# Kernel optimization log

Measured on AMD Instinct MI355X. Metric: run time of the kernel, lower is better.

The kernel has to match this reference:

```python
import jax, jax.numpy as jnp
import numpy as np

S = 4096  # source_sequence_size
Q = 4096  # query_sequence_size
E = 2048  # embedding_size
D = 2048  # output_embedding_size


def setup_inputs() -> dict:
    key = jax.random.key(0)
    ks = jax.random.split(key, 9)
    s = 1.0 / np.sqrt(E)
    return {
        "key": jax.random.normal(ks[0], (S, E), jnp.float32),
        "value": jax.random.normal(ks[1], (S, E), jnp.float32),
        "query": jax.random.normal(ks[2], (Q, E), jnp.float32),
        "Wk": jax.random.normal(ks[3], (D, E), jnp.float32) * s,
        "bk": jax.random.normal(ks[4], (D,), jnp.float32) * 0.01,
        "Wq": jax.random.normal(ks[5], (D, E), jnp.float32) * s,
        "bq": jax.random.normal(ks[6], (D,), jnp.float32) * 0.01,
        "Wv": jax.random.normal(ks[7], (D, E), jnp.float32) * s,
        "bv": jax.random.normal(ks[8], (D,), jnp.float32) * 0.01,
    }


def reference(key, value, query, Wk, bk, Wq, bq, Wv, bv):
    # Linear projections (nn.Linear: x @ W.T + b)
    k = key @ Wk.T + bk      # [S, D]
    v = value @ Wv.T + bv    # [S, D]
    q = query @ Wq.T + bq    # [Q, D]
    # Per-query-token attention scores over all source tokens (schema BOTH),
    # then weighted sum over value rows -- vectorized form of the per-token
    # apply_attention_scores loop.
    scale = 1.0 / jnp.sqrt(jnp.asarray(D, q.dtype))
    scores = jax.nn.softmax(jnp.einsum("qd,sd->qs", q, k) * scale, axis=-1)  # [Q, S]
    return jnp.einsum("qs,sd->qd", scores, v)  # [Q, D]
```

## Files before the change

kernel.cpp:

```cpp
#include <hip/hip_runtime.h>

#define S_SEQ 4096
#define Q_SEQ 4096
#define E_DIM 2048
#define D_DIM 2048

typedef __bf16 bf16;
typedef __bf16 bf16x4 __attribute__((ext_vector_type(4)));
typedef __bf16 bf16x8 __attribute__((ext_vector_type(8)));
typedef float f32x4 __attribute__((ext_vector_type(4)));

__global__ __launch_bounds__(256) void cast6(
    const float* __restrict__ i0, const float* __restrict__ i1,
    const float* __restrict__ i2, const float* __restrict__ i3,
    const float* __restrict__ i4, const float* __restrict__ i5,
    bf16* __restrict__ o0, bf16* __restrict__ o1, bf16* __restrict__ o2,
    bf16* __restrict__ o3, bf16* __restrict__ o4, bf16* __restrict__ o5) {
  const float* in;
  bf16* out;
  int n4;
  switch (blockIdx.y) {
    case 0: in = i0; out = o0; n4 = (S_SEQ * E_DIM) / 4; break;
    case 1: in = i1; out = o1; n4 = (S_SEQ * E_DIM) / 4; break;
    case 2: in = i2; out = o2; n4 = (S_SEQ * E_DIM) / 4; break;
    case 3: in = i3; out = o3; n4 = (D_DIM * E_DIM) / 4; break;
    case 4: in = i4; out = o4; n4 = (D_DIM * E_DIM) / 4; break;
    default: in = i5; out = o5; n4 = (D_DIM * E_DIM) / 4; break;
  }
  int i = blockIdx.x * 256 + threadIdx.x;
  if (i < n4) {
    float4 v = reinterpret_cast<const float4*>(in)[i];
    bf16x4 o;
    o[0] = (bf16)v.x; o[1] = (bf16)v.y; o[2] = (bf16)v.z; o[3] = (bf16)v.w;
    *reinterpret_cast<bf16x4*>(out + 4 * (size_t)i) = o;
  }
}

__device__ __forceinline__ void async_copy16(const bf16* g, bf16* l) {
  __builtin_amdgcn_global_load_lds(
      (const __attribute__((address_space(1))) void*)g,
      (__attribute__((address_space(3))) void*)l, 16, 0, 0);
}

__device__ __forceinline__ void xcd_remap32(int id, int nt, int& m, int& n) {
  int xcd = id & 7;
  int lid = id >> 3;
  m = (xcd & 3) * 8 + (lid & 7);
  n = (xcd >> 2) * (nt >> 1) + (lid >> 3);
}
__device__ __forceinline__ void xcd_remap16(int id, int nt, int& m, int& n) {
  int xcd = id & 7;
  int lid = id >> 3;
  m = (xcd & 3) * 4 + (lid & 3);
  n = (xcd >> 2) * (nt >> 1) + (lid >> 2);
}

template <int EPI>
__device__ __forceinline__ void gemm_body_sb(
    const bf16* __restrict__ A, int lda,
    const bf16* __restrict__ B, int ldb,
    void* __restrict__ C, int ldc,
    const float* __restrict__ aux, float scale, int K, int mBase, int nBase) {
  __shared__ __align__(16) bf16 Als[128 * 64];
  __shared__ __align__(16) bf16 Bls[128 * 64];

  const int tid  = threadIdx.x;
  const int wave = tid >> 6;
  const int lane = tid & 63;
  const int quad = lane >> 4;
  const int lrow = lane & 15;
  const int wRow = (wave >> 1) * 64;
  const int wCol = (wave & 1) * 64;

  f32x4 acc[4][4];
#pragma unroll
  for (int i = 0; i < 4; ++i)
#pragma unroll
    for (int j = 0; j < 4; ++j) {
      f32x4 z = {0.f, 0.f, 0.f, 0.f};
      acc[i][j] = z;
    }

  for (int k0 = 0; k0 < K; k0 += 64) {
#pragma unroll
    for (int c = 0; c < 4; ++c) {
      int chunk = c * 256 + tid;
      int row = chunk >> 3;
      int kc = (chunk & 7) ^ (row & 7);
      const bf16* g = A + (size_t)(mBase + row) * lda + k0 + kc * 8;
      async_copy16(g, Als + (size_t)(c * 256 + wave * 64) * 8);
    }
#pragma unroll
    for (int c = 0; c < 4; ++c) {
      int chunk = c * 256 + tid;
      int row = chunk >> 3;
      int kc = (chunk & 7) ^ (row & 7);
      const bf16* g = B + (size_t)(nBase + row) * ldb + k0 + kc * 8;
      async_copy16(g, Bls + (size_t)(c * 256 + wave * 64) * 8);
    }
    __syncthreads();

#pragma unroll
    for (int kk = 0; kk < 2; ++kk) {
      bf16x8 af[4], bfr[4];
#pragma unroll
      for (int i = 0; i < 4; ++i) {
        int r = wRow + i * 16 + lrow;
        int slot = (kk * 4 + quad) ^ (r & 7);
        af[i] = *(const bf16x8*)(Als + (size_t)r * 64 + slot * 8);
      }
#pragma unroll
      for (int j = 0; j < 4; ++j) {
        int r = wCol + j * 16 + lrow;
        int slot = (kk * 4 + quad) ^ (r & 7);
        bfr[j] = *(const bf16x8*)(Bls + (size_t)r * 64 + slot * 8);
      }
#pragma unroll
      for (int i = 0; i < 4; ++i)
#pragma unroll
        for (int j = 0; j < 4; ++j)
          acc[i][j] = __builtin_amdgcn_mfma_f32_16x16x32_bf16(af[i], bfr[j], acc[i][j], 0, 0, 0);
    }
    __syncthreads();
  }

#pragma unroll
  for (int j = 0; j < 4; ++j) {
    const int cn = nBase + wCol + j * 16 + lrow;
    float bj = 0.f;
    if (EPI == 0) bj = aux[cn];
#pragma unroll
    for (int i = 0; i < 4; ++i) {
      const int rbase = mBase + wRow + i * 16 + quad * 4;
#pragma unroll
      for (int r = 0; r < 4; ++r) {
        if (EPI == 0)
          ((bf16*)C)[(size_t)(rbase + r) * ldc + cn] = (bf16)(acc[i][j][r] + bj);
      }
    }
  }
}

template <int EPI>
__device__ __forceinline__ void gemm_body_c(
    const bf16* __restrict__ A, int lda,
    const bf16* __restrict__ B, int ldb,
    void* __restrict__ C, int ldc,
    float scale, int K, int mBase, int nBase,
    float* __restrict__ psum) {
  __shared__ __align__(16) bf16 Als[256 * 64];
  __shared__ __align__(16) bf16 Bls[128 * 64];

  const int tid  = threadIdx.x;
  const int wave = tid >> 6;
  const int lane = tid & 63;
  const int quad = lane >> 4;
  const int lrow = lane & 15;
  const int wRow = (wave >> 1) * 128;
  const int wCol = (wave & 1) * 64;

  f32x4 acc[8][4];
#pragma unroll
  for (int i = 0; i < 8; ++i)
#pragma unroll
    for (int j = 0; j < 4; ++j) {
      f32x4 z = {0.f, 0.f, 0.f, 0.f};
      acc[i][j] = z;
    }

  for (int k0 = 0; k0 < K; k0 += 64) {
#pragma unroll
    for (int c = 0; c < 8; ++c) {
      int chunk = c * 256 + tid;
      int row = chunk >> 3;
      int kc = (chunk & 7) ^ (row & 7);
      const bf16* g = A + (size_t)(mBase + row) * lda + k0 + kc * 8;
      async_copy16(g, Als + (size_t)(c * 256 + wave * 64) * 8);
    }
#pragma unroll
    for (int c = 0; c < 4; ++c) {
      int chunk = c * 256 + tid;
      int row = chunk >> 3;
      int kc = (chunk & 7) ^ (row & 7);
      const bf16* g = B + (size_t)(nBase + row) * ldb + k0 + kc * 8;
      async_copy16(g, Bls + (size_t)(c * 256 + wave * 64) * 8);
    }
    __syncthreads();

#pragma unroll
    for (int kk = 0; kk < 2; ++kk) {
      bf16x8 af[8], bfr[4];
#pragma unroll
      for (int i = 0; i < 8; ++i) {
        int r = wRow + i * 16 + lrow;
        int slot = (kk * 4 + quad) ^ (r & 7);
        af[i] = *(const bf16x8*)(Als + (size_t)r * 64 + slot * 8);
      }
#pragma unroll
      for (int j = 0; j < 4; ++j) {
        int r = wCol + j * 16 + lrow;
        int slot = (kk * 4 + quad) ^ (r & 7);
        bfr[j] = *(const bf16x8*)(Bls + (size_t)r * 64 + slot * 8);
      }
#pragma unroll
      for (int i = 0; i < 8; ++i)
#pragma unroll
        for (int j = 0; j < 4; ++j)
          acc[i][j] = __builtin_amdgcn_mfma_f32_16x16x32_bf16(af[i], bfr[j], acc[i][j], 0, 0, 0);
    }
    __syncthreads();
  }

  float sp[8][4];
#pragma unroll
  for (int i = 0; i < 8; ++i)
#pragma unroll
    for (int r = 0; r < 4; ++r) sp[i][r] = 0.f;
#pragma unroll
  for (int j = 0; j < 4; ++j) {
    const int cn = nBase + wCol + j * 16 + lrow;
#pragma unroll
    for (int i = 0; i < 8; ++i) {
      const int rbase = mBase + wRow + i * 16 + quad * 4;
#pragma unroll
      for (int r = 0; r < 4; ++r) {
        bf16 eb = (bf16)__expf(acc[i][j][r] * scale);
        ((bf16*)C)[(size_t)(rbase + r) * ldc + cn] = eb;
        sp[i][r] += (float)eb;
      }
    }
  }
#pragma unroll
  for (int i = 0; i < 8; ++i)
#pragma unroll
    for (int r = 0; r < 4; ++r) {
#pragma unroll
      for (int off = 1; off < 16; off <<= 1)
        sp[i][r] += __shfl_xor(sp[i][r], off, 64);
    }
  if (lrow == 0) {
    const int col64 = (nBase + wCol) >> 6;
#pragma unroll
    for (int i = 0; i < 8; ++i) {
      const int rbase = mBase + wRow + i * 16 + quad * 4;
#pragma unroll
      for (int r = 0; r < 4; ++r)
        psum[(size_t)(rbase + r) * 64 + col64] = sp[i][r];
    }
  }
}

__device__ __forceinline__ void stage_half(const bf16* __restrict__ G, int ld,
                                           int grow0, int k0, bf16* lds,
                                           int wave, int lane) {
#pragma unroll
  for (int s = 0; s < 2; ++s) {
    int c = (wave * 2 + s) * 64 + lane;
    int row = c >> 3;
    int kc = (c & 7) ^ (row & 7);
    const bf16* g = G + (size_t)(grow0 + row) * ld + k0 + kc * 8;
    async_copy16(g, lds + (size_t)(wave * 2 + s) * 512);
  }
}

#define BARRIER __builtin_amdgcn_s_barrier()
#define LGKM0 asm volatile("s_waitcnt lgkmcnt(0)" ::: "memory")
#define VMCNT2 asm volatile("s_waitcnt vmcnt(2)" ::: "memory")
#define VMCNT0 asm volatile("s_waitcnt vmcnt(0)" ::: "memory")

#define RD_A(buf, IP)                                                         \
  _Pragma("unroll") for (int ii = 0; ii < 2; ++ii)                            \
  _Pragma("unroll") for (int kk = 0; kk < 2; ++kk)                            \
      aR[ii][kk] = *(const bf16x8*)(&Als[buf][(size_t)(wRow + ((IP)*2 + ii) * 16 + lrow) * 64 + slotk[kk] * 8]);

#define RD_B(buf, JP, dst)                                                    \
  _Pragma("unroll") for (int jj = 0; jj < 2; ++jj)                            \
  _Pragma("unroll") for (int kk = 0; kk < 2; ++kk)                            \
      dst[jj][kk] = *(const bf16x8*)(&Bls[buf][(size_t)(wCol + ((JP)*2 + jj) * 16 + lrow) * 64 + slotk[kk] * 8]);

#define MMA16(IP)                                                              \
  __builtin_amdgcn_s_setprio(1);                                               \
  _Pragma("unroll") for (int jj = 0; jj < 2; ++jj)                             \
  _Pragma("unroll") for (int ii = 0; ii < 2; ++ii)                             \
  _Pragma("unroll") for (int kk = 0; kk < 2; ++kk)                             \
      acc[(IP)*2 + ii][jj] = __builtin_amdgcn_mfma_f32_16x16x32_bf16(          \
          aR[ii][kk], b0[jj][kk], acc[(IP)*2 + ii][jj], 0, 0, 0);              \
  _Pragma("unroll") for (int jj = 0; jj < 2; ++jj)                             \
  _Pragma("unroll") for (int ii = 0; ii < 2; ++ii)                             \
  _Pragma("unroll") for (int kk = 0; kk < 2; ++kk)                             \
      acc[(IP)*2 + ii][2 + jj] = __builtin_amdgcn_mfma_f32_16x16x32_bf16(      \
          aR[ii][kk], b1[jj][kk], acc[(IP)*2 + ii][2 + jj], 0, 0, 0);          \
  __builtin_amdgcn_s_setprio(0)

template <int EPI>
__device__ __forceinline__ void gemm_body_4ph(
    const bf16* __restrict__ A, int lda,
    const bf16* __restrict__ B, int ldb,
    void* __restrict__ C, int ldc,
    const float* __restrict__ aux, float scale, int K, int mBase, int nBase) {
  __shared__ __align__(16) bf16 Als[2][256 * 64];
  __shared__ __align__(16) bf16 Bls[2][128 * 64];

  const int tid  = threadIdx.x;
  const int wave = tid >> 6;
  const int lane = tid & 63;
  const int quad = lane >> 4;
  const int lrow = lane & 15;
  const int wRow = (wave >> 1) * 64;
  const int wCol = (wave & 1) * 64;
  const int slotk[2] = {quad ^ (lrow & 7), (4 + quad) ^ (lrow & 7)};

  f32x4 acc[4][4];
#pragma unroll
  for (int i = 0; i < 4; ++i)
#pragma unroll
    for (int j = 0; j < 4; ++j) {
      f32x4 z = {0.f, 0.f, 0.f, 0.f};
      acc[i][j] = z;
    }

  bf16x8 aR[2][2], b0[2][2], b1[2][2];

  stage_half(B, ldb, nBase, 0, &Bls[0][0], wave, lane);
  stage_half(A, lda, mBase, 0, &Als[0][0], wave, lane);
  stage_half(A, lda, mBase + 128, 0, &Als[0][128 * 64], wave, lane);
  stage_half(B, ldb, nBase, 64, &Bls[1][0], wave, lane);
  VMCNT2;
  BARRIER;

  const int NI = K >> 7;
#pragma unroll 1
  for (int i = 0; i < NI; ++i) {
    const bool nl = (i + 1 < NI);
    const int kb = i * 128;
    RD_A(0, 0);
    RD_B(0, 0, b0);
    RD_B(0, 1, b1);
    stage_half(A, lda, mBase, kb + 64, &Als[1][0], wave, lane);
    stage_half(A, lda, mBase + 128, kb + 64, &Als[1][128 * 64], wave, lane);
    BARRIER; LGKM0; MMA16(0); BARRIER;
    RD_A(0, 1);
    if (nl) {
      stage_half(B, ldb, nBase, kb + 128, &Bls[0][0], wave, lane);
      VMCNT2;
    } else {
      VMCNT0;
    }
    BARRIER; LGKM0; MMA16(1); BARRIER;
    RD_A(1, 0);
    RD_B(1, 0, b0);
    RD_B(1, 1, b1);
    if (nl) {
      stage_half(A, lda, mBase, kb + 128, &Als[0][0], wave, lane);
      stage_half(A, lda, mBase + 128, kb + 128, &Als[0][128 * 64], wave, lane);
    }
    BARRIER; LGKM0; MMA16(0); BARRIER;
    RD_A(1, 1);
    if (nl) {
      stage_half(B, ldb, nBase, kb + 192, &Bls[1][0], wave, lane);
      VMCNT2;
    }
    BARRIER; LGKM0; MMA16(1); BARRIER;
  }

  float rinv[4][4];
#pragma unroll
  for (int i = 0; i < 4; ++i)
#pragma unroll
    for (int r = 0; r < 4; ++r)
      rinv[i][r] = aux[mBase + wRow + i * 16 + quad * 4 + r];
#pragma unroll
  for (int j = 0; j < 4; ++j) {
    const int cn = nBase + wCol + j * 16 + lrow;
#pragma unroll
    for (int i = 0; i < 4; ++i) {
      const int rbase = mBase + wRow + i * 16 + quad * 4;
#pragma unroll
      for (int r = 0; r < 4; ++r)
        ((float*)C)[(size_t)(rbase + r) * ldc + cn] = acc[i][j][r] * rinv[i][r];
    }
  }
}

__global__ __launch_bounds__(256, 2) void qk_gemm(
    const bf16* __restrict__ A, const bf16* __restrict__ B,
    bf16* __restrict__ E, float scale,
    const bf16* __restrict__ v, bf16* __restrict__ vT,
    float* __restrict__ psum) {
  if (blockIdx.x >= 512) {
    __shared__ bf16 ttile[64][66];
    const int t = threadIdx.x;
    const int col = t & 63;
    const int r4 = t >> 6;
    const int base = (blockIdx.x - 512) * 4;
#pragma unroll 1
    for (int t4 = 0; t4 < 4; ++t4) {
      const int id = base + t4;
      const int c0 = (id & 31) * 64;
      const int r0 = (id >> 5) * 64;
#pragma unroll
      for (int i = 0; i < 16; ++i) {
        int rr = i * 4 + r4;
        ttile[rr][col] = v[(size_t)(r0 + rr) * D_DIM + c0 + col];
      }
      __syncthreads();
#pragma unroll
      for (int i = 0; i < 16; ++i) {
        int rr = i * 4 + r4;
        vT[(size_t)(c0 + rr) * S_SEQ + r0 + col] = ttile[col][rr];
      }
      __syncthreads();
    }
    return;
  }
  int m, n;
  xcd_remap16(blockIdx.x, 32, m, n);
  gemm_body_c<1>(A, D_DIM, B, D_DIM, (void*)E, S_SEQ, scale, D_DIM,
                 m * 256, n * 128, psum);
}

__global__ __launch_bounds__(512, 2) void pv_gemm(
    const bf16* __restrict__ E, const bf16* __restrict__ vT,
    float* __restrict__ out, const float* __restrict__ inv) {
  int m, n;
  xcd_remap16(blockIdx.x, 16, m, n);
  gemm_body_4ph<2>(E, S_SEQ, vT, S_SEQ, (void*)out, D_DIM, inv, 0.f, S_SEQ,
                   m * 256, n * 128);
}

__global__ __launch_bounds__(256, 2) void proj_gemm(
    const bf16* __restrict__ xk, const bf16* __restrict__ xq,
    const bf16* __restrict__ xv,
    const bf16* __restrict__ Wk, const bf16* __restrict__ Wq,
    const bf16* __restrict__ Wv,
    const float* __restrict__ bk, const float* __restrict__ bq,
    const float* __restrict__ bv,
    bf16* __restrict__ ok, bf16* __restrict__ oq, bf16* __restrict__ ov) {
  const bf16 *A, *W;
  const float* b;
  bf16* o;
  switch (blockIdx.z) {
    case 0: A = xk; W = Wk; b = bk; o = ok; break;
    case 1: A = xq; W = Wq; b = bq; o = oq; break;
    default: A = xv; W = Wv; b = bv; o = ov; break;
  }
  int m, n;
  xcd_remap32(blockIdx.x, 16, m, n);
  gemm_body_sb<0>(A, E_DIM, W, E_DIM, (void*)o, D_DIM, b, 0.f, E_DIM,
                  m * 128, n * 128);
}

__global__ __launch_bounds__(256) void rowsum2(
    const float* __restrict__ psum, float* __restrict__ inv) {
  const int r = blockIdx.x * 256 + threadIdx.x;
  const f32x4* p = (const f32x4*)(psum + (size_t)r * 64);
  float s = 0.f;
#pragma unroll
  for (int i = 0; i < 16; ++i) {
    f32x4 v = p[i];
    s += v[0] + v[1] + v[2] + v[3];
  }
  inv[r] = 1.0f / s;
}

extern "C" void kernel_launch(void* const* d_in, const int* in_sizes, int n_in,
                              void* d_out, int out_size, void* d_ws, size_t ws_size,
                              hipStream_t stream) {
  const float* key   = (const float*)d_in[0];
  const float* value = (const float*)d_in[1];
  const float* query = (const float*)d_in[2];
  const float* Wk = (const float*)d_in[3];
  const float* bk = (const float*)d_in[4];
  const float* Wq = (const float*)d_in[5];
  const float* bq = (const float*)d_in[6];
  const float* Wv = (const float*)d_in[7];
  const float* bv = (const float*)d_in[8];

  const size_t MB = 1ull << 20;
  char* ws = (char*)d_ws;
  bf16* key_bf   = (bf16*)(ws + 0 * MB);
  bf16* value_bf = (bf16*)(ws + 16 * MB);
  bf16* query_bf = (bf16*)(ws + 32 * MB);
  bf16* Wk_bf    = (bf16*)(ws + 48 * MB);
  bf16* Wq_bf    = (bf16*)(ws + 56 * MB);
  bf16* Wv_bf    = (bf16*)(ws + 64 * MB);
  bf16* k_bf     = (bf16*)(ws + 72 * MB);
  bf16* q_bf     = (bf16*)(ws + 88 * MB);
  bf16* v_bf     = (bf16*)(ws + 104 * MB);
  bf16* vT_bf    = (bf16*)(ws + 120 * MB);
  bf16* E        = (bf16*)(ws + 0 * MB);
  float* psum    = (float*)(ws + 34 * MB);
  float* inv     = (float*)(ws + 35 * MB);

  dim3 blk(256);
  dim3 blk512(512);

  cast6<<<dim3(8192, 6), blk, 0, stream>>>(
      key, value, query, Wk, Wq, Wv,
      key_bf, value_bf, query_bf, Wk_bf, Wq_bf, Wv_bf);

  proj_gemm<<<dim3(512, 1, 3), blk, 0, stream>>>(
      key_bf, query_bf, value_bf, Wk_bf, Wq_bf, Wv_bf, bk, bq, bv,
      k_bf, q_bf, v_bf);

  const float scale = 0.022097086912079608f;
  qk_gemm<<<dim3(1024), blk, 0, stream>>>(q_bf, k_bf, E, scale,
                                          v_bf, vT_bf, psum);

  rowsum2<<<dim3(16), blk, 0, stream>>>(psum, inv);

  pv_gemm<<<dim3(256), blk512, 0, stream>>>(E, vT_bf, (float*)d_out, inv);
}
```

Baseline: 419.2 us.

## Rewrite QK GEMM as 8-wave 256x256 double-buffered ping-pong pipeline

Replaces the single-buffered 256x128 QK^T GEMM (256 threads) with a 512-thread kernel. It uses a 256x256 tile, double-buffered LDS and interleaved async global-to-LDS staging between MFMA phases, gated by explicit vmcnt/lgkmcnt waits and barriers. The aim is to hide global load latency behind MFMA work and to get more reuse per tile. The V transpose that was folded into the extra blocks of qk_gemm now runs as its own kernel launch. This adds one launch and roughly doubles LDS per block, which may limit occupancy.

```diff
diff --git a/kernel.cpp b/kernel.cpp
--- a/kernel.cpp
+++ b/kernel.cpp
@@ -55,6 +55,24 @@
   n = (xcd >> 2) * (nt >> 1) + (lid >> 2);
 }
 
+__device__ __forceinline__ void stage_half(const bf16* __restrict__ G, int ld,
+                                           int grow0, int k0, bf16* lds,
+                                           int wave, int lane) {
+#pragma unroll
+  for (int s = 0; s < 2; ++s) {
+    int c = (wave * 2 + s) * 64 + lane;
+    int row = c >> 3;
+    int kc = (c & 7) ^ (row & 7);
+    const bf16* g = G + (size_t)(grow0 + row) * ld + k0 + kc * 8;
+    async_copy16(g, lds + (size_t)(wave * 2 + s) * 512);
+  }
+}
+
+#define BARRIER __builtin_amdgcn_s_barrier()
+#define LGKM0 asm volatile("s_waitcnt lgkmcnt(0)" ::: "memory")
+#define VMCNT2 asm volatile("s_waitcnt vmcnt(2)" ::: "memory")
+#define VMCNT0 asm volatile("s_waitcnt vmcnt(0)" ::: "memory")
+
 template <int EPI>
 __device__ __forceinline__ void gemm_body_sb(
     const bf16* __restrict__ A, int lda,
@@ -141,23 +159,27 @@
   }
 }
 
-template <int EPI>
-__device__ __forceinline__ void gemm_body_c(
-    const bf16* __restrict__ A, int lda,
-    const bf16* __restrict__ B, int ldb,
-    void* __restrict__ C, int ldc,
-    float scale, int K, int mBase, int nBase,
-    float* __restrict__ psum) {
-  __shared__ __align__(16) bf16 Als[256 * 64];
-  __shared__ __align__(16) bf16 Bls[128 * 64];
+__global__ __launch_bounds__(512, 2) void qk8_gemm(
+    const bf16* __restrict__ A, const bf16* __restrict__ B,
+    bf16* __restrict__ E, float scale, float* __restrict__ psum) {
+  __shared__ __align__(16) bf16 Als[2][256 * 64];
+  __shared__ __align__(16) bf16 Bls[2][256 * 64];
+
+  int m, n;
+  xcd_remap16(blockIdx.x, 16, m, n);
+  const int mBase = m * 256, nBase = n * 256;
+  const int lda = D_DIM, ldb = D_DIM, ldc = S_SEQ;
+  const int K = D_DIM;
 
   const int tid  = threadIdx.x;
   const int wave = tid >> 6;
   const int lane = tid & 63;
   const int quad = lane >> 4;
   const int lrow = lane & 15;
-  const int wRow = (wave >> 1) * 128;
-  const int wCol = (wave & 1) * 64;
+  const int wm = wave >> 2;
+  const int wn = wave & 3;
+  const int wRow = wm * 128;
+  const int wCol = wn * 64;
 
   f32x4 acc[8][4];
 #pragma unroll
@@ -168,47 +190,84 @@
       acc[i][j] = z;
     }
 
-  for (int k0 = 0; k0 < K; k0 += 64) {
-#pragma unroll
-    for (int c = 0; c < 8; ++c) {
-      int chunk = c * 256 + tid;
-      int row = chunk >> 3;
-      int kc = (chunk & 7) ^ (row & 7);
-      const bf16* g = A + (size_t)(mBase + row) * lda + k0 + kc * 8;
-      async_copy16(g, Als + (size_t)(c * 256 + wave * 64) * 8);
-    }
-#pragma unroll
-    for (int c = 0; c < 4; ++c) {
-      int chunk = c * 256 + tid;
-      int row = chunk >> 3;
-      int kc = (chunk & 7) ^ (row & 7);
-      const bf16* g = B + (size_t)(nBase + row) * ldb + k0 + kc * 8;
-      async_copy16(g, Bls + (size_t)(c * 256 + wave * 64) * 8);
-    }
-    __syncthreads();
-
-#pragma unroll
-    for (int kk = 0; kk < 2; ++kk) {
-      bf16x8 af[8], bfr[4];
-#pragma unroll
-      for (int i = 0; i < 8; ++i) {
-        int r = wRow + i * 16 + lrow;
+  bf16x8 aR[4][2], b0[2][2], b1[2][2];
+
+  auto rdA = [&](int buf, int QI) {
+#pragma unroll
+    for (int i = 0; i < 4; ++i)
+#pragma unroll
+      for (int kk = 0; kk < 2; ++kk) {
+        int r = wRow + QI * 64 + i * 16 + lrow;
         int slot = (kk * 4 + quad) ^ (r & 7);
-        af[i] = *(const bf16x8*)(Als + (size_t)r * 64 + slot * 8);
+        aR[i][kk] = *(const bf16x8*)(&Als[buf][(size_t)r * 64 + slot * 8]);
       }
-#pragma unroll
-      for (int j = 0; j < 4; ++j) {
-        int r = wCol + j * 16 + lrow;
+  };
+  auto rdB = [&](int buf, int JP, bf16x8 (&dst)[2][2]) {
+#pragma unroll
+    for (int j = 0; j < 2; ++j)
+#pragma unroll
+      for (int kk = 0; kk < 2; ++kk) {
+        int r = wCol + (JP * 2 + j) * 16 + lrow;
         int slot = (kk * 4 + quad) ^ (r & 7);
-        bfr[j] = *(const bf16x8*)(Bls + (size_t)r * 64 + slot * 8);
+        dst[j][kk] = *(const bf16x8*)(&Bls[buf][(size_t)r * 64 + slot * 8]);
       }
-#pragma unroll
-      for (int i = 0; i < 8; ++i)
-#pragma unroll
-        for (int j = 0; j < 4; ++j)
-          acc[i][j] = __builtin_amdgcn_mfma_f32_16x16x32_bf16(af[i], bfr[j], acc[i][j], 0, 0, 0);
-    }
-    __syncthreads();
+  };
+  auto mma = [&](int QI, int JP, bf16x8 (&bb)[2][2]) {
+    __builtin_amdgcn_s_setprio(1);
+#pragma unroll
+    for (int i = 0; i < 4; ++i)
+#pragma unroll
+      for (int j = 0; j < 2; ++j)
+#pragma unroll
+        for (int kk = 0; kk < 2; ++kk)
+          acc[QI * 4 + i][JP * 2 + j] = __builtin_amdgcn_mfma_f32_16x16x32_bf16(
+              aR[i][kk], bb[j][kk], acc[QI * 4 + i][JP * 2 + j], 0, 0, 0);
+    __builtin_amdgcn_s_setprio(0);
+  };
+
+  stage_half(A, lda, mBase,       0, &Als[0][0],        wave, lane);
+  stage_half(A, lda, mBase + 128, 0, &Als[0][128 * 64], wave, lane);
+  stage_half(B, ldb, nBase,       0, &Bls[0][0],        wave, lane);
+  stage_half(B, ldb, nBase + 128, 0, &Bls[0][128 * 64], wave, lane);
+  stage_half(A, lda, mBase,      64, &Als[1][0],        wave, lane);
+  VMCNT2;
+  BARRIER;
+
+  const int NI = K >> 7;
+#pragma unroll 1
+  for (int i = 0; i < NI; ++i) {
+    const bool nl = (i + 1 < NI);
+    const int kb = i * 128;
+    stage_half(A, lda, mBase + 128, kb + 64, &Als[1][128 * 64], wave, lane);
+    rdA(0, 0); rdB(0, 0, b0);
+    BARRIER; LGKM0; mma(0, 0, b0); BARRIER;
+    stage_half(B, ldb, nBase,       kb + 64, &Bls[1][0],        wave, lane);
+    rdB(0, 1, b1);
+    BARRIER; LGKM0; mma(0, 1, b1); BARRIER;
+    stage_half(B, ldb, nBase + 128, kb + 64, &Bls[1][128 * 64], wave, lane);
+    rdA(0, 1);
+    BARRIER; LGKM0; mma(1, 1, b1); BARRIER;
+    if (nl) {
+      stage_half(A, lda, mBase, kb + 128, &Als[0][0], wave, lane);
+      VMCNT2;
+    } else {
+      VMCNT0;
+    }
+    BARRIER; mma(1, 0, b0); BARRIER;
+    if (nl) stage_half(A, lda, mBase + 128, kb + 128, &Als[0][128 * 64], wave, lane);
+    rdA(1, 0); rdB(1, 0, b0);
+    BARRIER; LGKM0; mma(0, 0, b0); BARRIER;
+    if (nl) stage_half(B, ldb, nBase,       kb + 128, &Bls[0][0],        wave, lane);
+    rdB(1, 1, b1);
+    BARRIER; LGKM0; mma(0, 1, b1); BARRIER;
+    if (nl) stage_half(B, ldb, nBase + 128, kb + 128, &Bls[0][128 * 64], wave, lane);
+    rdA(1, 1);
+    BARRIER; LGKM0; mma(1, 1, b1); BARRIER;
+    if (nl) {
+      stage_half(A, lda, mBase, kb + 192, &Als[1][0], wave, lane);
+      VMCNT2;
+    }
+    BARRIER; mma(1, 0, b0); BARRIER;
   }
 
   float sp[8][4];
@@ -225,7 +284,7 @@
 #pragma unroll
       for (int r = 0; r < 4; ++r) {
         bf16 eb = (bf16)__expf(acc[i][j][r] * scale);
-        ((bf16*)C)[(size_t)(rbase + r) * ldc + cn] = eb;
+        E[(size_t)(rbase + r) * ldc + cn] = eb;
         sp[i][r] += (float)eb;
       }
     }
@@ -249,24 +308,6 @@
     }
   }
 }
-
-__device__ __forceinline__ void stage_half(const bf16* __restrict__ G, int ld,
-                                           int grow0, int k0, bf16* lds,
-                                           int wave, int lane) {
-#pragma unroll
-  for (int s = 0; s < 2; ++s) {
-    int c = (wave * 2 + s) * 64 + lane;
-    int row = c >> 3;
-    int kc = (c & 7) ^ (row & 7);
-    const bf16* g = G + (size_t)(grow0 + row) * ld + k0 + kc * 8;
-    async_copy16(g, lds + (size_t)(wave * 2 + s) * 512);
-  }
-}
-
-#define BARRIER __builtin_amdgcn_s_barrier()
-#define LGKM0 asm volatile("s_waitcnt lgkmcnt(0)" ::: "memory")
-#define VMCNT2 asm volatile("s_waitcnt vmcnt(2)" ::: "memory")
-#define VMCNT0 asm volatile("s_waitcnt vmcnt(0)" ::: "memory")
 
 #define RD_A(buf, IP)                                                         \
   _Pragma("unroll") for (int ii = 0; ii < 2; ++ii)                            \
@@ -382,43 +423,6 @@
   }
 }
 
-__global__ __launch_bounds__(256, 2) void qk_gemm(
-    const bf16* __restrict__ A, const bf16* __restrict__ B,
-    bf16* __restrict__ E, float scale,
-    const bf16* __restrict__ v, bf16* __restrict__ vT,
-    float* __restrict__ psum) {
-  if (blockIdx.x >= 512) {
-    __shared__ bf16 ttile[64][66];
-    const int t = threadIdx.x;
-    const int col = t & 63;
-    const int r4 = t >> 6;
-    const int base = (blockIdx.x - 512) * 4;
-#pragma unroll 1
-    for (int t4 = 0; t4 < 4; ++t4) {
-      const int id = base + t4;
-      const int c0 = (id & 31) * 64;
-      const int r0 = (id >> 5) * 64;
-#pragma unroll
-      for (int i = 0; i < 16; ++i) {
-        int rr = i * 4 + r4;
-        ttile[rr][col] = v[(size_t)(r0 + rr) * D_DIM + c0 + col];
-      }
-      __syncthreads();
-#pragma unroll
-      for (int i = 0; i < 16; ++i) {
-        int rr = i * 4 + r4;
-        vT[(size_t)(c0 + rr) * S_SEQ + r0 + col] = ttile[col][rr];
-      }
-      __syncthreads();
-    }
-    return;
-  }
-  int m, n;
-  xcd_remap16(blockIdx.x, 32, m, n);
-  gemm_body_c<1>(A, D_DIM, B, D_DIM, (void*)E, S_SEQ, scale, D_DIM,
-                 m * 256, n * 128, psum);
-}
-
 __global__ __launch_bounds__(512, 2) void pv_gemm(
     const bf16* __restrict__ E, const bf16* __restrict__ vT,
     float* __restrict__ out, const float* __restrict__ inv) {
@@ -450,6 +454,27 @@
                   m * 128, n * 128);
 }
 
+__global__ __launch_bounds__(256) void transpose_bf16(
+    const bf16* __restrict__ in, bf16* __restrict__ out) {
+  __shared__ bf16 tile[64][66];
+  const int t = threadIdx.x;
+  const int c0 = blockIdx.x * 64;
+  const int r0 = blockIdx.y * 64;
+  const int col = t & 63;
+  const int r4 = t >> 6;
+#pragma unroll
+  for (int i = 0; i < 16; ++i) {
+    int rr = i * 4 + r4;
+    tile[rr][col] = in[(size_t)(r0 + rr) * D_DIM + c0 + col];
+  }
+  __syncthreads();
+#pragma unroll
+  for (int i = 0; i < 16; ++i) {
+    int rr = i * 4 + r4;
+    out[(size_t)(c0 + rr) * S_SEQ + r0 + col] = tile[col][rr];
+  }
+}
+
 __global__ __launch_bounds__(256) void rowsum2(
     const float* __restrict__ psum, float* __restrict__ inv) {
   const int r = blockIdx.x * 256 + threadIdx.x;
@@ -503,9 +528,10 @@
       key_bf, query_bf, value_bf, Wk_bf, Wq_bf, Wv_bf, bk, bq, bv,
       k_bf, q_bf, v_bf);
 
+  transpose_bf16<<<dim3(D_DIM / 64, S_SEQ / 64), blk, 0, stream>>>(v_bf, vT_bf);
+
   const float scale = 0.022097086912079608f;
-  qk_gemm<<<dim3(1024), blk, 0, stream>>>(q_bf, k_bf, E, scale,
-                                          v_bf, vT_bf, psum);
+  qk8_gemm<<<dim3(256), blk512, 0, stream>>>(q_bf, k_bf, E, scale, psum);
 
   rowsum2<<<dim3(16), blk, 0, stream>>>(psum, inv);
 
```

Result: slower. 439.7 us (+4.9%).
